# Optimization experiments

Measured on AMD Instinct MI355X. Metric: run time of the kernel, lower is better.

The kernel has to match this reference:

```python
import jax, jax.numpy as jnp
import numpy as np

NIN = 1024
NOUT = 1024
NHEADS = 16
DHEAD = NOUT // NHEADS


def setup_inputs() -> dict:
    key = jax.random.key(0)
    k1, k2, k3, k4 = jax.random.split(key, 4)
    y = jax.random.normal(k1, (2, 2048, NIN), dtype=jnp.float32)
    Wqkv = jax.random.normal(k2, (NIN, 3 * NOUT), dtype=jnp.float32) * (1.0 / np.sqrt(NIN))
    Wff = jax.random.normal(k3, (NOUT, NOUT), dtype=jnp.float32) * (1.0 / np.sqrt(NOUT))
    bff = jax.random.normal(k4, (NOUT,), dtype=jnp.float32) * 0.01
    return {"y": y, "Wqkv": Wqkv, "Wff": Wff, "bff": bff}


def reference(y, Wqkv, Wff, bff):
    b, n, _ = y.shape
    qkv = y @ Wqkv  # [b, n, 3*nout]
    qkv = qkv.reshape(b, n, 3, NHEADS, DHEAD).transpose(2, 0, 3, 1, 4)
    q, k, v = qkv[0], qkv[1], qkv[2]  # each [b, h, n, d]
    att = jnp.einsum('bhqd,bhkd->bhqk', q, k)
    causal = jnp.triu(jnp.ones((n, n), dtype=bool), k=1)
    att = jnp.where(causal, -jnp.inf, att)
    att = jax.nn.softmax(att / jnp.sqrt(jnp.float32(DHEAD)), axis=-1)
    ctx = jnp.einsum('bhqk,bhkd->bhqd', att, v)
    ctx = ctx.transpose(0, 2, 1, 3).reshape(b, n, NOUT)
    return ctx @ Wff + bff
```

## Files before the change

kernel.cpp:

```cpp
#include <hip/hip_runtime.h>
#include <stdint.h>

#define NHEADS 16
#define DHEAD 64
#define SEQ 2048
#define BATCH 2
#define NINF 1024
#define NOUTF 1024
#define N3 3072
#define MTOT 4096

typedef unsigned short US;
typedef __attribute__((ext_vector_type(8))) short short8;
typedef __attribute__((ext_vector_type(4))) short short4v;
typedef __attribute__((ext_vector_type(4))) float f32x4;

__device__ inline US f2bf(float f) {
  union { float f; unsigned u; } v; v.f = f;
  unsigned r = v.u + 0x7fffu + ((v.u >> 16) & 1u);
  return (US)(r >> 16);
}

__device__ inline f32x4 mfma16(short8 a, short8 b, f32x4 c) {
  return __builtin_amdgcn_mfma_f32_16x16x32_bf16(a, b, c, 0, 0, 0);
}

__device__ inline f32x4 mfma16k16(short4v a, short4v b, f32x4 c) {
  return __builtin_amdgcn_mfma_f32_16x16x16bf16_1k(a, b, c, 0, 0, 0);
}

__device__ inline void async16(const US* g, US* l) {
  __builtin_amdgcn_global_load_lds(
      (const __attribute__((address_space(1))) unsigned int*)g,
      (__attribute__((address_space(3))) unsigned int*)l, 16, 0, 0);
}

__global__ void k_convert(const float* __restrict__ src, US* __restrict__ dst, int n4) {
  int i = blockIdx.x * blockDim.x + threadIdx.x;
  if (i >= n4) return;
  float4 v = ((const float4*)src)[i];
  ushort4 o;
  o.x = f2bf(v.x); o.y = f2bf(v.y); o.z = f2bf(v.z); o.w = f2bf(v.w);
  ((ushort4*)dst)[i] = o;
}

__global__ void k_wtrans(const float* __restrict__ Wqkv, const float* __restrict__ Wff,
                         US* __restrict__ dq, US* __restrict__ df) {
  __shared__ float tile[32][33];
  int bxi = blockIdx.x;
  const float* src; US* dst; int C;
  if (bxi < 96) { src = Wqkv; dst = dq; C = N3; }
  else          { src = Wff;  dst = df; C = NOUTF; bxi -= 96; }
  int bx = bxi * 32, by = blockIdx.y * 32;
  int tx = threadIdx.x, ty = threadIdx.y;
  for (int i = 0; i < 32; i += 8)
    tile[ty + i][tx] = src[(size_t)(by + ty + i) * C + bx + tx];
  __syncthreads();
  for (int i = 0; i < 32; i += 8)
    dst[(size_t)(bx + ty + i) * 1024 + by + tx] = f2bf(tile[tx][ty + i]);
}

__global__ void k_vtrans(const US* __restrict__ src, US* __restrict__ dst) {
  __shared__ US tile[32][33];
  int bh = blockIdx.z;
  int bx = blockIdx.x * 32;
  int by = blockIdx.y * 32;
  int tx = threadIdx.x, ty = threadIdx.y;
  const US* s0 = src + (size_t)bh * SEQ * DHEAD;
  US* d0 = dst + (size_t)bh * DHEAD * SEQ;
  for (int i = 0; i < 32; i += 8)
    tile[ty + i][tx] = s0[(size_t)(by + ty + i) * DHEAD + bx + tx];
  __syncthreads();
  for (int i = 0; i < 32; i += 8)
    d0[(size_t)(bx + ty + i) * SEQ + by + tx] = tile[tx][ty + i];
}

__global__ __launch_bounds__(256) void k_gemm_qkv(
    const US* __restrict__ A,
    const US* __restrict__ Bt,
    US* __restrict__ qbuf, US* __restrict__ kbuf, US* __restrict__ vbuf) {
  __shared__ US As[128 * 32];
  __shared__ US Bs[128 * 32];
  int tid = threadIdx.x;
  int wave = tid >> 6, lane = tid & 63, lm = lane & 15, lk = lane >> 4;
  int wm = wave >> 1, wn = wave & 1;
  int mbase = blockIdx.y * 128, nbase = blockIdx.x * 128;

  f32x4 acc[4][4];
#pragma unroll
  for (int i = 0; i < 4; ++i)
#pragma unroll
    for (int j = 0; j < 4; ++j) acc[i][j] = (f32x4){0.f, 0.f, 0.f, 0.f};

  const US* ga = A + (size_t)(mbase + (tid >> 2)) * NINF + (tid & 3) * 8;
  const US* gb = Bt + (size_t)(nbase + (tid >> 2)) * NINF + (tid & 3) * 8;
  US* la = As + tid * 8;
  US* lb = Bs + tid * 8;

  for (int kt = 0; kt < NINF / 32; ++kt) {
    int ko = kt * 32;
    async16(ga + ko, la);
    async16(ga + ko + (size_t)64 * NINF, la + 64 * 32);
    async16(gb + ko, lb);
    async16(gb + ko + (size_t)64 * NINF, lb + 64 * 32);
    __syncthreads();
    short8 a[4], b[4];
#pragma unroll
    for (int i = 0; i < 4; ++i)
      a[i] = *(const short8*)(As + (wm * 64 + i * 16 + lm) * 32 + lk * 8);
#pragma unroll
    for (int j = 0; j < 4; ++j)
      b[j] = *(const short8*)(Bs + (wn * 64 + j * 16 + lm) * 32 + lk * 8);
#pragma unroll
    for (int i = 0; i < 4; ++i)
#pragma unroll
      for (int j = 0; j < 4; ++j) acc[i][j] = mfma16(a[i], b[j], acc[i][j]);
    __syncthreads();
  }

  int which = nbase >> 10;
  US* dsts = (which == 0) ? qbuf : (which == 1) ? kbuf : vbuf;
  float sc = (which == 0) ? 0.18033688011112042f : 1.f;
#pragma unroll
  for (int j = 0; j < 4; ++j) {
    int col = nbase + wn * 64 + j * 16 + lm;
    int hh = (col & 1023) >> 6;
    int d = col & 63;
#pragma unroll
    for (int i = 0; i < 4; ++i) {
#pragma unroll
      for (int r = 0; r < 4; ++r) {
        int row = mbase + wm * 64 + i * 16 + lk * 4 + r;
        int bb = row >> 11;
        int s = row & (SEQ - 1);
        int bh = bb * NHEADS + hh;
        dsts[((size_t)bh * SEQ + s) * DHEAD + d] = f2bf(acc[i][j][r] * sc);
      }
    }
  }
}

__global__ __launch_bounds__(256) void k_attn(
    const US* __restrict__ qbuf, const US* __restrict__ kbuf,
    const US* __restrict__ vtbuf, US* __restrict__ ctx) {
  __shared__ US Ks[2][64 * 64];
  __shared__ US Vs[2][64 * 64];
  int tid = threadIdx.x;
  int w = tid >> 6, lane = tid & 63;
  int lm = lane & 15, lk = lane >> 4;
  int bl = blockIdx.x;
  int xcd = bl & 7, g = bl >> 3;
  int bh = (g & 3) * 8 + xcd;
  int q4 = g >> 2;
  int rr = q4 >> 3, qq = q4 & 7;
  int s = (rr == 0) ? 31 - qq : (rr == 1) ? qq : (rr == 2) ? 23 - qq : 8 + qq;
  int qb = s * 64 + w * 16;
  int nt = s + 1;

  const US* kbase = kbuf + (size_t)bh * SEQ * DHEAD;
  const US* vtb = vtbuf + (size_t)bh * DHEAD * SEQ;
  const US* qr = qbuf + ((size_t)bh * SEQ + qb + lm) * DHEAD + lk * 8;
  short8 qf0 = *(const short8*)(qr);
  short8 qf1 = *(const short8*)(qr + 32);

  int swz = ((lane & 7) ^ (lane >> 3)) * 8;
  const US* gsrc[4];
  US* ldst[4];
  int step[4];
#pragma unroll
  for (int j = 0; j < 4; ++j) {
    int u = w + 4 * j;
    if (u < 8) {
      gsrc[j] = kbase + (size_t)(u * 8 + (lane >> 3)) * DHEAD + swz;
      ldst[j] = &Ks[0][0] + u * 512 + lane * 8;
      step[j] = 64 * DHEAD;
    } else {
      int i = u - 8;
      gsrc[j] = vtb + (size_t)(i * 8 + (lane >> 3)) * SEQ + swz;
      ldst[j] = &Vs[0][0] + i * 512 + lane * 8;
      step[j] = 64;
    }
  }

  int xorv = lm & 7;
  int ck0 = ((lk) ^ xorv) * 16;
  int ck1 = ((4 + lk) ^ xorv) * 16;
  int cv[4];
#pragma unroll
  for (int kg = 0; kg < 4; ++kg)
    cv[kg] = (((kg * 2 + (lk >> 1)) ^ xorv) * 16) + (lk & 1) * 8;

  f32x4 o[4];
#pragma unroll
  for (int dg = 0; dg < 4; ++dg) o[dg] = (f32x4){0.f, 0.f, 0.f, 0.f};
  f32x4 lacc = (f32x4){0.f, 0.f, 0.f, 0.f};
  const short4v kones = {(short)0x3F80, (short)0x3F80, (short)0x3F80, (short)0x3F80};

  auto body = [&](const char* Kc, const char* Vc, int kg, bool dm) {
    const char* kr = Kc + (kg * 16 + lm) * 128;
    short8 ka0 = *(const short8*)(kr + ck0);
    short8 ka1 = *(const short8*)(kr + ck1);
    f32x4 st = (f32x4){0.f, 0.f, 0.f, 0.f};
    st = mfma16(ka0, qf0, st);
    st = mfma16(ka1, qf1, st);
    uint32_t ue[4];
#pragma unroll
    for (int r = 0; r < 4; ++r) {
      float v = st[r];
      if (dm && (lk * 4 + r > lm)) v = -INFINITY;
      union { float f; uint32_t u; } cv2;
      cv2.f = exp2f(v);
      ue[r] = cv2.u + 0x8000u;
    }
    union { short4v s4; uint32_t u[2]; } pk;
    pk.u[0] = __builtin_amdgcn_perm(ue[1], ue[0], 0x07060302u);
    pk.u[1] = __builtin_amdgcn_perm(ue[3], ue[2], 0x07060302u);
    lacc = mfma16k16(kones, pk.s4, lacc);
    const char* vr = Vc + lm * 128 + cv[kg];
#pragma unroll
    for (int dg = 0; dg < 4; ++dg) {
      short4v va = *(const short4v*)(vr + dg * 2048);
      o[dg] = mfma16k16(va, pk.s4, o[dg]);
    }
  };

#pragma unroll
  for (int j = 0; j < 4; ++j) { async16(gsrc[j], ldst[j]); gsrc[j] += step[j]; }
  if (nt > 1) {
#pragma unroll
    for (int j = 0; j < 4; ++j) { async16(gsrc[j], ldst[j] + 4096); gsrc[j] += step[j]; }
  }

  for (int t = 0; t < nt; ++t) {
    if (t + 1 < nt) asm volatile("s_waitcnt vmcnt(4)" ::: "memory");
    else            asm volatile("s_waitcnt vmcnt(0)" ::: "memory");
    __builtin_amdgcn_s_barrier();
    asm volatile("" ::: "memory");
    const char* Kc = (const char*)Ks + (t & 1) * 8192;
    const char* Vc = (const char*)Vs + (t & 1) * 8192;
    if (t < s) {
#pragma unroll
      for (int kg = 0; kg < 4; ++kg) body(Kc, Vc, kg, false);
    } else {
      for (int kg = 0; kg < w; ++kg) body(Kc, Vc, kg, false);
      body(Kc, Vc, w, true);
    }
    asm volatile("" ::: "memory");
    __builtin_amdgcn_s_barrier();
    asm volatile("" ::: "memory");
    if (t + 2 < nt) {
#pragma unroll
      for (int j = 0; j < 4; ++j) {
        async16(gsrc[j], ldst[j] + (t & 1) * 4096);
        gsrc[j] += step[j];
      }
    }
  }

  float inv = 1.f / lacc[0];

  US* crow = ctx + ((size_t)(bh >> 4) * SEQ + qb + lm) * NOUTF + (bh & 15) * DHEAD;
#pragma unroll
  for (int dg = 0; dg < 4; ++dg) {
    union { short4v s4; uint32_t u[2]; } pk;
    pk.u[0] = (uint32_t)f2bf(o[dg][0] * inv) | ((uint32_t)f2bf(o[dg][1] * inv) << 16);
    pk.u[1] = (uint32_t)f2bf(o[dg][2] * inv) | ((uint32_t)f2bf(o[dg][3] * inv) << 16);
    *(short4v*)(crow + dg * 16 + lk * 4) = pk.s4;
  }
}

__global__ __launch_bounds__(256) void k_gemm_out(
    const US* __restrict__ A, const US* __restrict__ Bt,
    const float* __restrict__ bias, float* __restrict__ out) {
  __shared__ US As[128 * 32];
  __shared__ US Bs[64 * 32];
  int tid = threadIdx.x;
  int wave = tid >> 6, lane = tid & 63, lm = lane & 15, lk = lane >> 4;
  int mbase = blockIdx.y * 128, nbase = blockIdx.x * 64;

  f32x4 acc[2][4];
#pragma unroll
  for (int i = 0; i < 2; ++i)
#pragma unroll
    for (int j = 0; j < 4; ++j) acc[i][j] = (f32x4){0.f, 0.f, 0.f, 0.f};

  const US* ga = A + (size_t)(mbase + (tid >> 2)) * NOUTF + (tid & 3) * 8;
  const US* gb = Bt + (size_t)(nbase + (tid >> 2)) * NOUTF + (tid & 3) * 8;
  US* la = As + tid * 8;
  US* lb = Bs + tid * 8;

  for (int kt = 0; kt < NOUTF / 32; ++kt) {
    int ko = kt * 32;
    async16(ga + ko, la);
    async16(ga + ko + (size_t)64 * NOUTF, la + 64 * 32);
    async16(gb + ko, lb);
    __syncthreads();
    short8 a[2], b[4];
#pragma unroll
    for (int i = 0; i < 2; ++i)
      a[i] = *(const short8*)(As + (wave * 32 + i * 16 + lm) * 32 + lk * 8);
#pragma unroll
    for (int j = 0; j < 4; ++j)
      b[j] = *(const short8*)(Bs + (j * 16 + lm) * 32 + lk * 8);
#pragma unroll
    for (int i = 0; i < 2; ++i)
#pragma unroll
      for (int j = 0; j < 4; ++j) acc[i][j] = mfma16(a[i], b[j], acc[i][j]);
    __syncthreads();
  }

#pragma unroll
  for (int j = 0; j < 4; ++j) {
    int col = nbase + j * 16 + lm;
    float bv = bias[col];
#pragma unroll
    for (int i = 0; i < 2; ++i)
#pragma unroll
      for (int r = 0; r < 4; ++r) {
        int row = mbase + wave * 32 + i * 16 + lk * 4 + r;
        out[(size_t)row * NOUTF + col] = acc[i][j][r] + bv;
      }
  }
}

extern "C" void kernel_launch(void* const* d_in, const int* in_sizes, int n_in,
                              void* d_out, int out_size, void* d_ws, size_t ws_size,
                              hipStream_t stream) {
  const float* y    = (const float*)d_in[0];
  const float* Wqkv = (const float*)d_in[1];
  const float* Wff  = (const float*)d_in[2];
  const float* bff  = (const float*)d_in[3];
  float* out = (float*)d_out;

  char* ws = (char*)d_ws;
  US* ybf   = (US*)(ws);
  US* ctx   = (US*)(ws);
  US* wqkvt = (US*)(ws + (8u << 20));
  US* wfft  = (US*)(ws + (14u << 20));
  US* qbuf  = (US*)(ws + (16u << 20));
  US* kbuf  = (US*)(ws + (24u << 20));
  US* vbuf  = (US*)(ws + (32u << 20));
  US* vtbuf = (US*)(ws + (40u << 20));

  k_convert<<<MTOT * NINF / 4 / 256, 256, 0, stream>>>(y, ybf, MTOT * NINF / 4);
  k_wtrans<<<dim3(128, 32), dim3(32, 8), 0, stream>>>(Wqkv, Wff, wqkvt, wfft);
  k_gemm_qkv<<<dim3(N3 / 128, MTOT / 128), 256, 0, stream>>>(ybf, wqkvt, qbuf, kbuf, vbuf);
  k_vtrans<<<dim3(DHEAD / 32, SEQ / 32, BATCH * NHEADS), dim3(32, 8), 0, stream>>>(vbuf, vtbuf);
  k_attn<<<dim3(1024), 256, 0, stream>>>(qbuf, kbuf, vtbuf, ctx);
  k_gemm_out<<<dim3(NOUTF / 64, MTOT / 128), 256, 0, stream>>>(ctx, wfft, bff, out);
}
```

Before: 184.1 us.

## Split attention work across waves by key sub-block and reduce partial outputs in LDS

Each wave used to own 16 query rows and walk every key block. Now each wave owns one 16-key slice of every 64-key tile and computes partial outputs for all 64 query rows. The partial outputs and row sums are then summed across waves through shared memory after the loop. Row sums move from an MFMA with a ones vector to scalar adds, and s_setprio is raised around the compute section. This cuts per-wave LDS reads of K and V and balances the diagonal-block work, at the cost of 4x more accumulator registers and an added end-of-kernel reduction with barriers.

Measured after the change: 200.1 us. 8.7% more time.

```diff
diff --git a/kernel.cpp b/kernel.cpp
--- a/kernel.cpp
+++ b/kernel.cpp
@@ -143,8 +143,9 @@
 __global__ __launch_bounds__(256) void k_attn(
     const US* __restrict__ qbuf, const US* __restrict__ kbuf,
     const US* __restrict__ vtbuf, US* __restrict__ ctx) {
-  __shared__ US Ks[2][64 * 64];
-  __shared__ US Vs[2][64 * 64];
+  __shared__ __align__(16) char smem[32768];
+  US* KsB = (US*)smem;
+  US* VsB = (US*)(smem + 16384);
   int tid = threadIdx.x;
   int w = tid >> 6, lane = tid & 63;
   int lm = lane & 15, lk = lane >> 4;
@@ -152,16 +153,20 @@
   int xcd = bl & 7, g = bl >> 3;
   int bh = (g & 3) * 8 + xcd;
   int q4 = g >> 2;
-  int rr = q4 >> 3, qq = q4 & 7;
-  int s = (rr == 0) ? 31 - qq : (rr == 1) ? qq : (rr == 2) ? 23 - qq : 8 + qq;
-  int qb = s * 64 + w * 16;
+  int rnd = q4 >> 3, qq = q4 & 7;
+  int s = (rnd == 0) ? 31 - qq : (rnd == 1) ? qq : (rnd == 2) ? 23 - qq : 8 + qq;
   int nt = s + 1;
 
   const US* kbase = kbuf + (size_t)bh * SEQ * DHEAD;
   const US* vtb = vtbuf + (size_t)bh * DHEAD * SEQ;
-  const US* qr = qbuf + ((size_t)bh * SEQ + qb + lm) * DHEAD + lk * 8;
-  short8 qf0 = *(const short8*)(qr);
-  short8 qf1 = *(const short8*)(qr + 32);
+
+  short8 qf[4][2];
+#pragma unroll
+  for (int qg = 0; qg < 4; ++qg) {
+    const US* qr = qbuf + ((size_t)bh * SEQ + s * 64 + qg * 16 + lm) * DHEAD + lk * 8;
+    qf[qg][0] = *(const short8*)(qr);
+    qf[qg][1] = *(const short8*)(qr + 32);
+  }
 
   int swz = ((lane & 7) ^ (lane >> 3)) * 8;
   const US* gsrc[4];
@@ -172,12 +177,12 @@
     int u = w + 4 * j;
     if (u < 8) {
       gsrc[j] = kbase + (size_t)(u * 8 + (lane >> 3)) * DHEAD + swz;
-      ldst[j] = &Ks[0][0] + u * 512 + lane * 8;
+      ldst[j] = KsB + u * 512 + lane * 8;
       step[j] = 64 * DHEAD;
     } else {
       int i = u - 8;
       gsrc[j] = vtb + (size_t)(i * 8 + (lane >> 3)) * SEQ + swz;
-      ldst[j] = &Vs[0][0] + i * 512 + lane * 8;
+      ldst[j] = VsB + i * 512 + lane * 8;
       step[j] = 64;
     }
   }
@@ -185,44 +190,14 @@
   int xorv = lm & 7;
   int ck0 = ((lk) ^ xorv) * 16;
   int ck1 = ((4 + lk) ^ xorv) * 16;
-  int cv[4];
-#pragma unroll
-  for (int kg = 0; kg < 4; ++kg)
-    cv[kg] = (((kg * 2 + (lk >> 1)) ^ xorv) * 16) + (lk & 1) * 8;
-
-  f32x4 o[4];
-#pragma unroll
-  for (int dg = 0; dg < 4; ++dg) o[dg] = (f32x4){0.f, 0.f, 0.f, 0.f};
-  f32x4 lacc = (f32x4){0.f, 0.f, 0.f, 0.f};
-  const short4v kones = {(short)0x3F80, (short)0x3F80, (short)0x3F80, (short)0x3F80};
-
-  auto body = [&](const char* Kc, const char* Vc, int kg, bool dm) {
-    const char* kr = Kc + (kg * 16 + lm) * 128;
-    short8 ka0 = *(const short8*)(kr + ck0);
-    short8 ka1 = *(const short8*)(kr + ck1);
-    f32x4 st = (f32x4){0.f, 0.f, 0.f, 0.f};
-    st = mfma16(ka0, qf0, st);
-    st = mfma16(ka1, qf1, st);
-    uint32_t ue[4];
-#pragma unroll
-    for (int r = 0; r < 4; ++r) {
-      float v = st[r];
-      if (dm && (lk * 4 + r > lm)) v = -INFINITY;
-      union { float f; uint32_t u; } cv2;
-      cv2.f = exp2f(v);
-      ue[r] = cv2.u + 0x8000u;
-    }
-    union { short4v s4; uint32_t u[2]; } pk;
-    pk.u[0] = __builtin_amdgcn_perm(ue[1], ue[0], 0x07060302u);
-    pk.u[1] = __builtin_amdgcn_perm(ue[3], ue[2], 0x07060302u);
-    lacc = mfma16k16(kones, pk.s4, lacc);
-    const char* vr = Vc + lm * 128 + cv[kg];
-#pragma unroll
-    for (int dg = 0; dg < 4; ++dg) {
-      short4v va = *(const short4v*)(vr + dg * 2048);
-      o[dg] = mfma16k16(va, pk.s4, o[dg]);
-    }
-  };
+  int cvw = (((w * 2 + (lk >> 1)) ^ xorv) * 16) + (lk & 1) * 8;
+
+  f32x4 o[4][4];
+#pragma unroll
+  for (int dg = 0; dg < 4; ++dg)
+#pragma unroll
+    for (int qg = 0; qg < 4; ++qg) o[dg][qg] = (f32x4){0.f, 0.f, 0.f, 0.f};
+  float racc[4] = {0.f, 0.f, 0.f, 0.f};
 
 #pragma unroll
   for (int j = 0; j < 4; ++j) { async16(gsrc[j], ldst[j]); gsrc[j] += step[j]; }
@@ -236,15 +211,49 @@
     else            asm volatile("s_waitcnt vmcnt(0)" ::: "memory");
     __builtin_amdgcn_s_barrier();
     asm volatile("" ::: "memory");
-    const char* Kc = (const char*)Ks + (t & 1) * 8192;
-    const char* Vc = (const char*)Vs + (t & 1) * 8192;
-    if (t < s) {
-#pragma unroll
-      for (int kg = 0; kg < 4; ++kg) body(Kc, Vc, kg, false);
-    } else {
-      for (int kg = 0; kg < w; ++kg) body(Kc, Vc, kg, false);
-      body(Kc, Vc, w, true);
-    }
+
+    const char* Kc = (const char*)(KsB + (t & 1) * 4096);
+    const char* Vc = (const char*)(VsB + (t & 1) * 4096);
+    bool diag = (t == s);
+
+    __builtin_amdgcn_s_setprio(1);
+    const char* kr = Kc + (w * 16 + lm) * 128;
+    short8 ka0 = *(const short8*)(kr + ck0);
+    short8 ka1 = *(const short8*)(kr + ck1);
+    short4v va[4];
+#pragma unroll
+    for (int dg = 0; dg < 4; ++dg)
+      va[dg] = *(const short4v*)(Vc + lm * 128 + cvw + dg * 2048);
+
+#pragma unroll
+    for (int qg = 0; qg < 4; ++qg) {
+      if (diag && qg < w) continue;
+      f32x4 st = (f32x4){0.f, 0.f, 0.f, 0.f};
+      st = mfma16(ka0, qf[qg][0], st);
+      st = mfma16(ka1, qf[qg][1], st);
+      bool pm = diag && (qg == w);
+      uint32_t ue[4];
+#pragma unroll
+      for (int r = 0; r < 4; ++r) {
+        float v = st[r];
+        if (pm && (lk * 4 + r > lm)) v = -INFINITY;
+        union { float f; uint32_t u; } cv2;
+        cv2.f = exp2f(v);
+        ue[r] = cv2.u + 0x8000u;
+      }
+      union { float f; uint32_t u; } b0, b1, b2, b3;
+      b0.u = ue[0] & 0xFFFF0000u; b1.u = ue[1] & 0xFFFF0000u;
+      b2.u = ue[2] & 0xFFFF0000u; b3.u = ue[3] & 0xFFFF0000u;
+      racc[qg] += (b0.f + b1.f) + (b2.f + b3.f);
+      union { short4v s4; uint32_t u[2]; } pk;
+      pk.u[0] = __builtin_amdgcn_perm(ue[1], ue[0], 0x07060302u);
+      pk.u[1] = __builtin_amdgcn_perm(ue[3], ue[2], 0x07060302u);
+#pragma unroll
+      for (int dg = 0; dg < 4; ++dg)
+        o[dg][qg] = mfma16k16(va[dg], pk.s4, o[dg][qg]);
+    }
+    __builtin_amdgcn_s_setprio(0);
+
     asm volatile("" ::: "memory");
     __builtin_amdgcn_s_barrier();
     asm volatile("" ::: "memory");
@@ -257,15 +266,51 @@
     }
   }
 
-  float inv = 1.f / lacc[0];
-
-  US* crow = ctx + ((size_t)(bh >> 4) * SEQ + qb + lm) * NOUTF + (bh & 15) * DHEAD;
-#pragma unroll
-  for (int dg = 0; dg < 4; ++dg) {
-    union { short4v s4; uint32_t u[2]; } pk;
-    pk.u[0] = (uint32_t)f2bf(o[dg][0] * inv) | ((uint32_t)f2bf(o[dg][1] * inv) << 16);
-    pk.u[1] = (uint32_t)f2bf(o[dg][2] * inv) | ((uint32_t)f2bf(o[dg][3] * inv) << 16);
-    *(short4v*)(crow + dg * 16 + lk * 4) = pk.s4;
+  f32x4* red4 = (f32x4*)smem;
+  f32x4* r4 = (f32x4*)(smem + 24 * 1024);
+#pragma unroll
+  for (int h = 0; h < 2; ++h) {
+#pragma unroll
+    for (int qg = 0; qg < 4; ++qg) {
+      if (qg != w) {
+        int c = (w < qg) ? w : w - 1;
+        red4[(qg * 3 + c) * 128 + 0 * 64 + lane] = o[h * 2 + 0][qg];
+        red4[(qg * 3 + c) * 128 + 1 * 64 + lane] = o[h * 2 + 1][qg];
+      }
+    }
+    if (h == 0) r4[w * 64 + lane] = (f32x4){racc[0], racc[1], racc[2], racc[3]};
+    __syncthreads();
+#pragma unroll
+    for (int qg = 0; qg < 4; ++qg) {
+      if (qg == w) {
+#pragma unroll
+        for (int c = 0; c < 3; ++c) {
+          o[h * 2 + 0][qg] += red4[(qg * 3 + c) * 128 + 0 * 64 + lane];
+          o[h * 2 + 1][qg] += red4[(qg * 3 + c) * 128 + 1 * 64 + lane];
+        }
+      }
+    }
+    __syncthreads();
+  }
+  const float* rr = (const float*)(smem + 24 * 1024);
+  float myrs = rr[(0 * 64 + lane) * 4 + w] + rr[(1 * 64 + lane) * 4 + w] +
+               rr[(2 * 64 + lane) * 4 + w] + rr[(3 * 64 + lane) * 4 + w];
+  myrs += __shfl_xor(myrs, 16);
+  myrs += __shfl_xor(myrs, 32);
+  float inv = 1.f / myrs;
+
+  US* crow = ctx + ((size_t)(bh >> 4) * SEQ + s * 64 + w * 16 + lm) * NOUTF + (bh & 15) * DHEAD;
+#pragma unroll
+  for (int qg = 0; qg < 4; ++qg) {
+    if (qg == w) {
+#pragma unroll
+      for (int dg = 0; dg < 4; ++dg) {
+        union { short4v s4; uint32_t u[2]; } pk;
+        pk.u[0] = (uint32_t)f2bf(o[dg][qg][0] * inv) | ((uint32_t)f2bf(o[dg][qg][1] * inv) << 16);
+        pk.u[1] = (uint32_t)f2bf(o[dg][qg][2] * inv) | ((uint32_t)f2bf(o[dg][qg][3] * inv) << 16);
+        *(short4v*)(crow + dg * 16 + lk * 4) = pk.s4;
+      }
+    }
   }
 }
 
```

## Split attention work across waves by query pairs and key halves with LDS reduction

Applied to the files above, without the earlier changes.

Each wave now owns two 16-row query groups and half of the 64-key tile, instead of one query group and all keys. K and V fragments loaded from LDS are reused across both query groups, which halves per-wave LDS reads. It also balances the causal diagonal tile, which previously gave uneven work to each wave. Partial outputs and row sums from the two key halves are combined through shared memory at the end, at the cost of an extra reduction, a sync, and more accumulator registers.

Result: no change. 181.2 us (-1.6%).

```diff
diff --git a/kernel.cpp b/kernel.cpp
--- a/kernel.cpp
+++ b/kernel.cpp
@@ -148,20 +148,26 @@
   int tid = threadIdx.x;
   int w = tid >> 6, lane = tid & 63;
   int lm = lane & 15, lk = lane >> 4;
+  int h = w >> 1;
+  int kh = w & 1;
   int bl = blockIdx.x;
   int xcd = bl & 7, g = bl >> 3;
   int bh = (g & 3) * 8 + xcd;
   int q4 = g >> 2;
-  int rr = q4 >> 3, qq = q4 & 7;
-  int s = (rr == 0) ? 31 - qq : (rr == 1) ? qq : (rr == 2) ? 23 - qq : 8 + qq;
-  int qb = s * 64 + w * 16;
+  int rnd = q4 >> 3, qq = q4 & 7;
+  int s = (rnd == 0) ? 31 - qq : (rnd == 1) ? qq : (rnd == 2) ? 23 - qq : 8 + qq;
   int nt = s + 1;
 
   const US* kbase = kbuf + (size_t)bh * SEQ * DHEAD;
   const US* vtb = vtbuf + (size_t)bh * DHEAD * SEQ;
-  const US* qr = qbuf + ((size_t)bh * SEQ + qb + lm) * DHEAD + lk * 8;
-  short8 qf0 = *(const short8*)(qr);
-  short8 qf1 = *(const short8*)(qr + 32);
+
+  short8 qf[2][2];
+#pragma unroll
+  for (int i = 0; i < 2; ++i) {
+    const US* qr = qbuf + ((size_t)bh * SEQ + s * 64 + (2 * h + i) * 16 + lm) * DHEAD + lk * 8;
+    qf[i][0] = *(const short8*)(qr);
+    qf[i][1] = *(const short8*)(qr + 32);
+  }
 
   int swz = ((lane & 7) ^ (lane >> 3)) * 8;
   const US* gsrc[4];
@@ -185,44 +191,20 @@
   int xorv = lm & 7;
   int ck0 = ((lk) ^ xorv) * 16;
   int ck1 = ((4 + lk) ^ xorv) * 16;
-  int cv[4];
-#pragma unroll
-  for (int kg = 0; kg < 4; ++kg)
-    cv[kg] = (((kg * 2 + (lk >> 1)) ^ xorv) * 16) + (lk & 1) * 8;
-
-  f32x4 o[4];
-#pragma unroll
-  for (int dg = 0; dg < 4; ++dg) o[dg] = (f32x4){0.f, 0.f, 0.f, 0.f};
-  f32x4 lacc = (f32x4){0.f, 0.f, 0.f, 0.f};
+  int cv[2];
+#pragma unroll
+  for (int kgi = 0; kgi < 2; ++kgi) {
+    int kg = 2 * kh + kgi;
+    cv[kgi] = (((kg * 2 + (lk >> 1)) ^ xorv) * 16) + (lk & 1) * 8;
+  }
+
+  f32x4 o[4][2];
+#pragma unroll
+  for (int dg = 0; dg < 4; ++dg)
+#pragma unroll
+    for (int i = 0; i < 2; ++i) o[dg][i] = (f32x4){0.f, 0.f, 0.f, 0.f};
+  f32x4 lacc[2] = {(f32x4){0.f, 0.f, 0.f, 0.f}, (f32x4){0.f, 0.f, 0.f, 0.f}};
   const short4v kones = {(short)0x3F80, (short)0x3F80, (short)0x3F80, (short)0x3F80};
-
-  auto body = [&](const char* Kc, const char* Vc, int kg, bool dm) {
-    const char* kr = Kc + (kg * 16 + lm) * 128;
-    short8 ka0 = *(const short8*)(kr + ck0);
-    short8 ka1 = *(const short8*)(kr + ck1);
-    f32x4 st = (f32x4){0.f, 0.f, 0.f, 0.f};
-    st = mfma16(ka0, qf0, st);
-    st = mfma16(ka1, qf1, st);
-    uint32_t ue[4];
-#pragma unroll
-    for (int r = 0; r < 4; ++r) {
-      float v = st[r];
-      if (dm && (lk * 4 + r > lm)) v = -INFINITY;
-      union { float f; uint32_t u; } cv2;
-      cv2.f = exp2f(v);
-      ue[r] = cv2.u + 0x8000u;
-    }
-    union { short4v s4; uint32_t u[2]; } pk;
-    pk.u[0] = __builtin_amdgcn_perm(ue[1], ue[0], 0x07060302u);
-    pk.u[1] = __builtin_amdgcn_perm(ue[3], ue[2], 0x07060302u);
-    lacc = mfma16k16(kones, pk.s4, lacc);
-    const char* vr = Vc + lm * 128 + cv[kg];
-#pragma unroll
-    for (int dg = 0; dg < 4; ++dg) {
-      short4v va = *(const short4v*)(vr + dg * 2048);
-      o[dg] = mfma16k16(va, pk.s4, o[dg]);
-    }
-  };
 
 #pragma unroll
   for (int j = 0; j < 4; ++j) { async16(gsrc[j], ldst[j]); gsrc[j] += step[j]; }
@@ -236,15 +218,49 @@
     else            asm volatile("s_waitcnt vmcnt(0)" ::: "memory");
     __builtin_amdgcn_s_barrier();
     asm volatile("" ::: "memory");
+
     const char* Kc = (const char*)Ks + (t & 1) * 8192;
     const char* Vc = (const char*)Vs + (t & 1) * 8192;
-    if (t < s) {
-#pragma unroll
-      for (int kg = 0; kg < 4; ++kg) body(Kc, Vc, kg, false);
-    } else {
-      for (int kg = 0; kg < w; ++kg) body(Kc, Vc, kg, false);
-      body(Kc, Vc, w, true);
-    }
+    bool diag = (t == s);
+
+#pragma unroll
+    for (int kgi = 0; kgi < 2; ++kgi) {
+      int kg = 2 * kh + kgi;
+      const char* kr = Kc + (kg * 16 + lm) * 128;
+      short8 ka0 = *(const short8*)(kr + ck0);
+      short8 ka1 = *(const short8*)(kr + ck1);
+      const char* vr = Vc + lm * 128 + cv[kgi];
+      short4v va[4];
+#pragma unroll
+      for (int dg = 0; dg < 4; ++dg)
+        va[dg] = *(const short4v*)(vr + dg * 2048);
+#pragma unroll
+      for (int i = 0; i < 2; ++i) {
+        int qg = 2 * h + i;
+        if (diag && kg > qg) continue;
+        f32x4 st = (f32x4){0.f, 0.f, 0.f, 0.f};
+        st = mfma16(ka0, qf[i][0], st);
+        st = mfma16(ka1, qf[i][1], st);
+        bool pm = diag && (kg == qg);
+        uint32_t ue[4];
+#pragma unroll
+        for (int r = 0; r < 4; ++r) {
+          float v = st[r];
+          if (pm && (lk * 4 + r > lm)) v = -INFINITY;
+          union { float f; uint32_t u; } cv2;
+          cv2.f = exp2f(v);
+          ue[r] = cv2.u + 0x8000u;
+        }
+        union { short4v s4; uint32_t u[2]; } pk;
+        pk.u[0] = __builtin_amdgcn_perm(ue[1], ue[0], 0x07060302u);
+        pk.u[1] = __builtin_amdgcn_perm(ue[3], ue[2], 0x07060302u);
+        lacc[i] = mfma16k16(kones, pk.s4, lacc[i]);
+#pragma unroll
+        for (int dg = 0; dg < 4; ++dg)
+          o[dg][i] = mfma16k16(va[dg], pk.s4, o[dg][i]);
+      }
+    }
+
     asm volatile("" ::: "memory");
     __builtin_amdgcn_s_barrier();
     asm volatile("" ::: "memory");
@@ -257,15 +273,34 @@
     }
   }
 
-  float inv = 1.f / lacc[0];
-
-  US* crow = ctx + ((size_t)(bh >> 4) * SEQ + qb + lm) * NOUTF + (bh & 15) * DHEAD;
-#pragma unroll
-  for (int dg = 0; dg < 4; ++dg) {
-    union { short4v s4; uint32_t u[2]; } pk;
-    pk.u[0] = (uint32_t)f2bf(o[dg][0] * inv) | ((uint32_t)f2bf(o[dg][1] * inv) << 16);
-    pk.u[1] = (uint32_t)f2bf(o[dg][2] * inv) | ((uint32_t)f2bf(o[dg][3] * inv) << 16);
-    *(short4v*)(crow + dg * 16 + lk * 4) = pk.s4;
+  f32x4* red4 = (f32x4*)&Ks[0][0];
+  f32x4* rl4 = (f32x4*)&Vs[0][0];
+  if (kh == 1) {
+#pragma unroll
+    for (int i = 0; i < 2; ++i) {
+#pragma unroll
+      for (int dg = 0; dg < 4; ++dg)
+        red4[((h * 2 + i) * 4 + dg) * 64 + lane] = o[dg][i];
+      rl4[(h * 2 + i) * 64 + lane] = lacc[i];
+    }
+  }
+  __syncthreads();
+  if (kh == 0) {
+#pragma unroll
+    for (int i = 0; i < 2; ++i) {
+      f32x4 ls = lacc[i] + rl4[(h * 2 + i) * 64 + lane];
+      float inv = 1.f / ls[0];
+      US* crow = ctx + ((size_t)(bh >> 4) * SEQ + s * 64 + (2 * h + i) * 16 + lm) * NOUTF +
+                 (bh & 15) * DHEAD;
+#pragma unroll
+      for (int dg = 0; dg < 4; ++dg) {
+        f32x4 oo = o[dg][i] + red4[((h * 2 + i) * 4 + dg) * 64 + lane];
+        union { short4v s4; uint32_t u[2]; } pk;
+        pk.u[0] = (uint32_t)f2bf(oo[0] * inv) | ((uint32_t)f2bf(oo[1] * inv) << 16);
+        pk.u[1] = (uint32_t)f2bf(oo[2] * inv) | ((uint32_t)f2bf(oo[3] * inv) << 16);
+        *(short4v*)(crow + dg * 16 + lk * 4) = pk.s4;
+      }
+    }
   }
 }
 
```

## Fuse V transpose into QKV GEMM epilogue and vectorize GEMM stores

Applied to the files above, without the earlier changes.

The QKV GEMM now writes V directly in transposed [bh, d, seq] layout, which removes the separate k_vtrans kernel and its extra round trip through global memory. For Q/K and the output GEMM, the MFMA operands are swapped so each lane holds four consecutive columns, letting the epilogues issue packed 8-byte bf16 stores and float4 stores with float4 bias loads in place of scalar ones. This adds a branch on the column block inside the K loop and changes the accumulator layout per output type.

After: 192.9 us. 1.05x slower.

```diff
diff --git a/kernel.cpp b/kernel.cpp
--- a/kernel.cpp
+++ b/kernel.cpp
@@ -60,31 +60,17 @@
     dst[(size_t)(bx + ty + i) * 1024 + by + tx] = f2bf(tile[tx][ty + i]);
 }
 
-__global__ void k_vtrans(const US* __restrict__ src, US* __restrict__ dst) {
-  __shared__ US tile[32][33];
-  int bh = blockIdx.z;
-  int bx = blockIdx.x * 32;
-  int by = blockIdx.y * 32;
-  int tx = threadIdx.x, ty = threadIdx.y;
-  const US* s0 = src + (size_t)bh * SEQ * DHEAD;
-  US* d0 = dst + (size_t)bh * DHEAD * SEQ;
-  for (int i = 0; i < 32; i += 8)
-    tile[ty + i][tx] = s0[(size_t)(by + ty + i) * DHEAD + bx + tx];
-  __syncthreads();
-  for (int i = 0; i < 32; i += 8)
-    d0[(size_t)(bx + ty + i) * SEQ + by + tx] = tile[tx][ty + i];
-}
-
 __global__ __launch_bounds__(256) void k_gemm_qkv(
     const US* __restrict__ A,
     const US* __restrict__ Bt,
-    US* __restrict__ qbuf, US* __restrict__ kbuf, US* __restrict__ vbuf) {
+    US* __restrict__ qbuf, US* __restrict__ kbuf, US* __restrict__ vtbuf) {
   __shared__ US As[128 * 32];
   __shared__ US Bs[128 * 32];
   int tid = threadIdx.x;
   int wave = tid >> 6, lane = tid & 63, lm = lane & 15, lk = lane >> 4;
   int wm = wave >> 1, wn = wave & 1;
   int mbase = blockIdx.y * 128, nbase = blockIdx.x * 128;
+  int which = nbase >> 10;
 
   f32x4 acc[4][4];
 #pragma unroll
@@ -111,30 +97,52 @@
 #pragma unroll
     for (int j = 0; j < 4; ++j)
       b[j] = *(const short8*)(Bs + (wn * 64 + j * 16 + lm) * 32 + lk * 8);
-#pragma unroll
-    for (int i = 0; i < 4; ++i)
-#pragma unroll
-      for (int j = 0; j < 4; ++j) acc[i][j] = mfma16(a[i], b[j], acc[i][j]);
+    if (which != 2) {
+#pragma unroll
+      for (int i = 0; i < 4; ++i)
+#pragma unroll
+        for (int j = 0; j < 4; ++j) acc[i][j] = mfma16(b[j], a[i], acc[i][j]);
+    } else {
+#pragma unroll
+      for (int i = 0; i < 4; ++i)
+#pragma unroll
+        for (int j = 0; j < 4; ++j) acc[i][j] = mfma16(a[i], b[j], acc[i][j]);
+    }
     __syncthreads();
   }
 
-  int which = nbase >> 10;
-  US* dsts = (which == 0) ? qbuf : (which == 1) ? kbuf : vbuf;
-  float sc = (which == 0) ? 0.18033688011112042f : 1.f;
-#pragma unroll
-  for (int j = 0; j < 4; ++j) {
-    int col = nbase + wn * 64 + j * 16 + lm;
-    int hh = (col & 1023) >> 6;
-    int d = col & 63;
+  int hh = ((nbase + wn * 64) & 1023) >> 6;
+  if (which != 2) {
+    US* dsts = (which == 0) ? qbuf : kbuf;
+    float sc = (which == 0) ? 0.18033688011112042f : 1.f;
 #pragma unroll
     for (int i = 0; i < 4; ++i) {
-#pragma unroll
-      for (int r = 0; r < 4; ++r) {
-        int row = mbase + wm * 64 + i * 16 + lk * 4 + r;
-        int bb = row >> 11;
-        int s = row & (SEQ - 1);
-        int bh = bb * NHEADS + hh;
-        dsts[((size_t)bh * SEQ + s) * DHEAD + d] = f2bf(acc[i][j][r] * sc);
+      int row = mbase + wm * 64 + i * 16 + lm;
+      int bh = (row >> 11) * NHEADS + hh;
+      int s = row & (SEQ - 1);
+      US* base = dsts + ((size_t)bh * SEQ + s) * DHEAD;
+#pragma unroll
+      for (int j = 0; j < 4; ++j) {
+        int d0 = j * 16 + lk * 4;
+        uint32_t lo = (uint32_t)f2bf(acc[i][j][0] * sc) | ((uint32_t)f2bf(acc[i][j][1] * sc) << 16);
+        uint32_t hi = (uint32_t)f2bf(acc[i][j][2] * sc) | ((uint32_t)f2bf(acc[i][j][3] * sc) << 16);
+        uint2 pv; pv.x = lo; pv.y = hi;
+        *(uint2*)(base + d0) = pv;
+      }
+    }
+  } else {
+#pragma unroll
+    for (int j = 0; j < 4; ++j) {
+      int d = j * 16 + lm;
+#pragma unroll
+      for (int i = 0; i < 4; ++i) {
+        int row0 = mbase + wm * 64 + i * 16 + lk * 4;
+        int bh = (row0 >> 11) * NHEADS + hh;
+        int s0 = row0 & (SEQ - 1);
+        uint32_t lo = (uint32_t)f2bf(acc[i][j][0]) | ((uint32_t)f2bf(acc[i][j][1]) << 16);
+        uint32_t hi = (uint32_t)f2bf(acc[i][j][2]) | ((uint32_t)f2bf(acc[i][j][3]) << 16);
+        uint2 pv; pv.x = lo; pv.y = hi;
+        *(uint2*)(vtbuf + ((size_t)bh * DHEAD + d) * SEQ + s0) = pv;
       }
     }
   }
@@ -152,8 +160,8 @@
   int xcd = bl & 7, g = bl >> 3;
   int bh = (g & 3) * 8 + xcd;
   int q4 = g >> 2;
-  int rr = q4 >> 3, qq = q4 & 7;
-  int s = (rr == 0) ? 31 - qq : (rr == 1) ? qq : (rr == 2) ? 23 - qq : 8 + qq;
+  int rnd = q4 >> 3, qq = q4 & 7;
+  int s = (rnd == 0) ? 31 - qq : (rnd == 1) ? qq : (rnd == 2) ? 23 - qq : 8 + qq;
   int qb = s * 64 + w * 16;
   int nt = s + 1;
 
@@ -305,21 +313,24 @@
 #pragma unroll
     for (int i = 0; i < 2; ++i)
 #pragma unroll
-      for (int j = 0; j < 4; ++j) acc[i][j] = mfma16(a[i], b[j], acc[i][j]);
+      for (int j = 0; j < 4; ++j) acc[i][j] = mfma16(b[j], a[i], acc[i][j]);
     __syncthreads();
   }
 
 #pragma unroll
   for (int j = 0; j < 4; ++j) {
-    int col = nbase + j * 16 + lm;
-    float bv = bias[col];
-#pragma unroll
-    for (int i = 0; i < 2; ++i)
-#pragma unroll
-      for (int r = 0; r < 4; ++r) {
-        int row = mbase + wave * 32 + i * 16 + lk * 4 + r;
-        out[(size_t)row * NOUTF + col] = acc[i][j][r] + bv;
-      }
+    int n0 = nbase + j * 16 + lk * 4;
+    float4 bv = *(const float4*)(bias + n0);
+#pragma unroll
+    for (int i = 0; i < 2; ++i) {
+      int row = mbase + wave * 32 + i * 16 + lm;
+      float4 ov;
+      ov.x = acc[i][j][0] + bv.x;
+      ov.y = acc[i][j][1] + bv.y;
+      ov.z = acc[i][j][2] + bv.z;
+      ov.w = acc[i][j][3] + bv.w;
+      *(float4*)(out + (size_t)row * NOUTF + n0) = ov;
+    }
   }
 }
 
@@ -339,13 +350,11 @@
   US* wfft  = (US*)(ws + (14u << 20));
   US* qbuf  = (US*)(ws + (16u << 20));
   US* kbuf  = (US*)(ws + (24u << 20));
-  US* vbuf  = (US*)(ws + (32u << 20));
   US* vtbuf = (US*)(ws + (40u << 20));
 
   k_convert<<<MTOT * NINF / 4 / 256, 256, 0, stream>>>(y, ybf, MTOT * NINF / 4);
   k_wtrans<<<dim3(128, 32), dim3(32, 8), 0, stream>>>(Wqkv, Wff, wqkvt, wfft);
-  k_gemm_qkv<<<dim3(N3 / 128, MTOT / 128), 256, 0, stream>>>(ybf, wqkvt, qbuf, kbuf, vbuf);
-  k_vtrans<<<dim3(DHEAD / 32, SEQ / 32, BATCH * NHEADS), dim3(32, 8), 0, stream>>>(vbuf, vtbuf);
+  k_gemm_qkv<<<dim3(N3 / 128, MTOT / 128), 256, 0, stream>>>(ybf, wqkvt, qbuf, kbuf, vtbuf);
   k_attn<<<dim3(1024), 256, 0, stream>>>(qbuf, kbuf, vtbuf, ctx);
   k_gemm_out<<<dim3(NOUTF / 64, MTOT / 128), 256, 0, stream>>>(ctx, wfft, bff, out);
 }
```
